# Performance work log

Measured on AMD Instinct MI355X. Metric: run time of the kernel, lower is better.

The kernel has to match this reference:

```python
import jax, jax.numpy as jnp
import numpy as np

NQ = 12          # num_qubits
NL = 5           # num_layers
NA = 4           # num_actions
DIM = 2 ** NQ    # state-vector dimension

# PennyLane convention: wire 0 is the most-significant bit of the state index.
_idx = np.arange(DIM)
_bits = (_idx[:, None] >> (NQ - 1 - np.arange(NQ))) & 1           # [DIM, NQ]
_cz = np.ones(DIM)
for _i in range(NQ):                                              # ring of CZs (all diagonal -> fuse)
    _cz *= np.where((_bits[:, _i] & _bits[:, (_i + 1) % NQ]) == 1, -1.0, 1.0)
CZ_RING = jnp.asarray(_cz, dtype=jnp.complex64)                   # [DIM]
ZTAB = jnp.asarray(1 - 2 * _bits[:, :NA], dtype=jnp.float32)      # [DIM, NA] PauliZ eigenvalues


def _bc(v):
    # broadcast an angle-derived scalar or [B] vector against [B, lead, trail]
    v = jnp.asarray(v)
    return v.reshape(v.shape + (1, 1))


def _apply_1q(state, wire, m00, m01, m10, m11):
    b = state.shape[0]
    lead, trail = 2 ** wire, 2 ** (NQ - 1 - wire)
    s = state.reshape(b, lead, 2, trail)
    s0, s1 = s[:, :, 0, :], s[:, :, 1, :]
    return jnp.stack([m00 * s0 + m01 * s1, m10 * s0 + m11 * s1], axis=2).reshape(b, DIM)


def _rx(state, wire, theta):
    c = _bc(jnp.cos(0.5 * theta)).astype(jnp.complex64)
    s = _bc(jnp.sin(0.5 * theta)).astype(jnp.complex64)
    return _apply_1q(state, wire, c, -1j * s, -1j * s, c)


def _ry(state, wire, theta):
    c = _bc(jnp.cos(0.5 * theta)).astype(jnp.complex64)
    s = _bc(jnp.sin(0.5 * theta)).astype(jnp.complex64)
    return _apply_1q(state, wire, c, -s, s, c)


def _rz(state, wire, theta):
    # diagonal gate: no mixing across the wire axis
    b = state.shape[0]
    lead, trail = 2 ** wire, 2 ** (NQ - 1 - wire)
    e = _bc(jnp.exp(-0.5j * theta))  # e^{-i t/2}; conj(e) = e^{+i t/2} for real t
    s = state.reshape(b, lead, 2, trail)
    return jnp.stack([e * s[:, :, 0, :], jnp.conj(e) * s[:, :, 1, :]], axis=2).reshape(b, DIM)


def setup_inputs() -> dict:
    key = jax.random.key(0)
    k1, k2 = jax.random.split(key)
    x = jax.random.normal(k1, (4096, 4 * NQ), dtype=jnp.float32)
    input_scaling = jnp.ones((NL, 3, NQ), dtype=jnp.float32)
    weights = jax.random.uniform(k2, (NL, 3, 2 * NQ), dtype=jnp.float32,
                                 minval=-np.pi, maxval=np.pi)
    output_scaling = jnp.ones((NA,), dtype=jnp.float32)
    return {"x": x, "input_scaling": input_scaling, "weights": weights,
            "output_scaling": output_scaling}


def reference(x, input_scaling, weights, output_scaling):
    b = x.shape[0]
    feats = (x[:, NQ:2 * NQ], x[:, 2 * NQ:3 * NQ], x[:, 3 * NQ:4 * NQ])
    state = jnp.zeros((b, DIM), dtype=jnp.complex64).at[:, 0].set(1.0)
    for layer in range(NL):
        for blk in range(3):
            f = feats[blk]
            for i in range(NQ):
                state = _rx(state, i, input_scaling[layer, blk, i] * f[:, i])
            for i in range(NQ):
                state = _ry(state, i, weights[layer, blk, i])
            for i in range(NQ):
                state = _rz(state, i, weights[layer, blk, i + NQ])
            state = state * CZ_RING[None, :]
    probs = state.real ** 2 + state.imag ** 2          # [B, DIM]
    expvals = probs @ ZTAB                             # [B, NA] <Z_i>
    return expvals * output_scaling                    # logits
```

## Files before the change

### kernel.cpp

```cpp
#include <hip/hip_runtime.h>
#include <stdint.h>

#define NQ 12
#define NL 5
#define NIT 15
#define AMPS 16
#define CPB (NIT * NQ)


typedef float f2 __attribute__((ext_vector_type(2)));

static __device__ __forceinline__ float f_u(unsigned u) { return __uint_as_float(u); }
static __device__ __forceinline__ unsigned u_f(float f) { return __float_as_uint(f); }

#define PK_MUL_RR(acc, C, S) \
    asm("v_pk_mul_f32 %0, %1, %2 op_sel_hi:[0,1]" : "=v"(acc) : "v"(C), "v"(S))
#define PK_FMA_I(acc, C, S) \
    asm("v_pk_fma_f32 %0, %1, %2, %0 op_sel:[1,1,0] op_sel_hi:[1,0,1] neg_lo:[1,0,0]" \
        : "+v"(acc) : "v"(C), "v"(S))
#define PK_FMA_R(acc, C, S) \
    asm("v_pk_fma_f32 %0, %1, %2, %0 op_sel_hi:[0,1,1]" : "+v"(acc) : "v"(C), "v"(S))
#define PK_FMA_IC(acc, C, S) \
    asm("v_pk_fma_f32 %0, %1, %2, %0 op_sel:[1,1,0] op_sel_hi:[1,0,1] neg_hi:[1,0,0]" \
        : "+v"(acc) : "v"(C), "v"(S))
#define PK_FMA_RN(acc, C, S) \
    asm("v_pk_fma_f32 %0, %1, %2, %0 op_sel_hi:[0,1,1] neg_lo:[1,0,0] neg_hi:[1,0,0]" \
        : "+v"(acc) : "v"(C), "v"(S))

#define CPLX_AB(DST, CA, S, CB, O)                                    \
    { f2 t_;                                                          \
      PK_MUL_RR(t_, CA, S); PK_FMA_I(t_, CA, S);                      \
      PK_FMA_R (t_, CB, O); PK_FMA_I(t_, CB, O);                      \
      DST = t_; }

template <int CTRL>
static __device__ __forceinline__ float dpp_xor(float v) {
    int u = (int)__float_as_uint(v);
    return __uint_as_float((unsigned)__builtin_amdgcn_update_dpp(u, u, CTRL, 0xF, 0xF, false));
}
static __device__ __forceinline__ float swz_xor4(float v) {
    return f_u((unsigned)__builtin_amdgcn_ds_swizzle((int)u_f(v), 0x101F));
}

#define AB_GATE_PK(OPX)                                                 \
    _Pragma("unroll")                                                   \
    for (int r = 0; r < AMPS; ++r) {                                    \
        f2 o; o.x = OPX(s[r].x); o.y = OPX(s[r].y);                     \
        CPLX_AB(s[r], CA, s[r], CB, o)                                  \
    }

template <int ST>
static __device__ __forceinline__ void reg_gate_pk(f2 (&s)[AMPS], f2 CAg, f2 CBg) {
#pragma unroll
    for (int r0 = 0; r0 < AMPS; ++r0) {
        if (r0 & ST) continue;
        const int r1 = r0 | ST;
        const f2 s0 = s[r0], s1 = s[r1];
        f2 t0, t1;
        PK_MUL_RR(t0, CAg, s0); PK_FMA_I (t0, CAg, s0);
        PK_FMA_R (t0, CBg, s1); PK_FMA_I (t0, CBg, s1);
        PK_MUL_RR(t1, CAg, s1); PK_FMA_IC(t1, CAg, s1);
        PK_FMA_RN(t1, CBg, s0); PK_FMA_I (t1, CBg, s0);
        s[r0] = t0; s[r1] = t1;
    }
}

static __device__ __forceinline__ float4 build_coef(float alpha, float beta, float gamma) {
    float sa, ca, sb, cb, sg, cg;
    sincosf(0.5f * alpha, &sa, &ca);
    sincosf(0.5f * beta,  &sb, &cb);
    sincosf(0.5f * gamma, &sg, &cg);
    float cbca = cb * ca, sbsa = sb * sa, sbca = sb * ca, cbsa = cb * sa;
    float ar =  cg * cbca + sg * sbsa;
    float ai =  cg * sbsa - sg * cbca;
    float br = -(cg * sbca + sg * cbsa);
    float bi =  sg * sbca - cg * cbsa;
    return make_float4(ar, ai, br, bi);
}

__global__ __launch_bounds__(256) void coef_kernel(
    const float* __restrict__ x, const float* __restrict__ iscale,
    const float* __restrict__ w, float4* __restrict__ ctab, int total)
{
    int gid = blockIdx.x * 256 + threadIdx.x;
    if (gid >= total) return;
    int b  = gid / CPB;
    int t  = gid - b * CPB;
    int it = t / NQ;
    int q  = t - it * NQ;
    int blk = it - 3 * (it / 3);
    float f     = x[(size_t)b * (4 * NQ) + NQ + blk * NQ + q];
    float alpha = iscale[it * NQ + q] * f;
    ctab[gid] = build_coef(alpha, w[it * 2 * NQ + q], w[it * 2 * NQ + NQ + q]);
}

template <bool TAB>
__global__ __launch_bounds__(256) void qsim_kernel(
    const float* __restrict__ x,
    const float* __restrict__ iscale,
    const float* __restrict__ w,
    const float* __restrict__ oscale,
    const float4* __restrict__ ctab,
    float* __restrict__ out)
{
    const int tid  = threadIdx.x;
    const int lane = tid & 63;
    const int wv   = tid >> 6;
    const int b    = blockIdx.x;

    extern __shared__ float4 smem[];
    float4* buf  = smem;
    float4* clds = smem + 1536;

#define TBUF(SLOT, Q) buf[((((SLOT) << 1) | (Q)) << 6) | lane]

    if constexpr (!TAB) {
        if (tid < CPB) {
            const int it  = tid / NQ;
            const int q   = tid - it * NQ;
            const int blk = it - 3 * (it / 3);
            float f     = x[(size_t)b * (4 * NQ) + NQ + blk * NQ + q];
            float alpha = iscale[it * NQ + q] * f;
            clds[tid] = build_coef(alpha, w[it * 2 * NQ + q], w[it * 2 * NQ + NQ + q]);
        }
        __syncthreads();
    }

    f2 s[AMPS];
#pragma unroll
    for (int r = 0; r < AMPS; ++r) { s[r].x = 0.f; s[r].y = 0.f; }
    if (tid == 0) s[0].x = 1.f;

    unsigned czmA = 0, czmB = 0;
#pragma unroll
    for (int r = 0; r < AMPS; ++r) {
        unsigned ia = ((unsigned)wv << 10) | ((unsigned)lane << 4) | (unsigned)r;
        unsigned ib = (((unsigned)(r >> 3) & 1u) << 11) | (((unsigned)(r >> 2) & 1u) << 10)
                    | ((unsigned)lane << 4)
                    | (((unsigned)(wv >> 1) & 1u) << 3) | (((unsigned)wv & 1u) << 2)
                    | ((unsigned)r & 3u);
        unsigned pa = ((unsigned)__popc((ia & (ia >> 1)) & 0x7FFu) + ((ia & (ia >> 11)) & 1u)) & 1u;
        unsigned pb = ((unsigned)__popc((ib & (ib >> 1)) & 0x7FFu) + ((ib & (ib >> 11)) & 1u)) & 1u;
        czmA |= pa << r;
        czmB |= pb << r;
    }

    const bool hb2 = (lane >> 5) & 1;
    const bool hb3 = (lane >> 4) & 1;
    const unsigned sb4 = (unsigned)((lane >> 3) & 1) << 31;
    const unsigned sb5 = (unsigned)((lane >> 2) & 1) << 31;
    const unsigned sb6 = (unsigned)((lane >> 1) & 1) << 31;
    const unsigned sb7 = (unsigned)(lane & 1) << 31;

    const float4* gtab = TAB ? (ctab + (size_t)b * CPB) : nullptr;

    float4 c[NQ];
    if constexpr (TAB) {
#pragma unroll
        for (int q = 0; q < NQ; ++q) c[q] = gtab[q];
    } else {
#pragma unroll
        for (int q = 0; q < NQ; ++q) c[q] = clds[q];
    }

#pragma unroll 1
    for (int it = 0; it < NIT; ++it) {
        float4 cn[NQ];
        if constexpr (TAB) {
            const float4* nxt = gtab + (it + 1 < NIT ? (it + 1) * NQ : it * NQ);
#pragma unroll
            for (int q = 0; q < NQ; ++q) cn[q] = nxt[q];
        } else {
            const float4* nxt = clds + (it + 1 < NIT ? (it + 1) * NQ : it * NQ);
#pragma unroll
            for (int q = 0; q < NQ; ++q) cn[q] = nxt[q];
        }

        const bool ev = (it & 1) == 0;

        {
            const float4 c0 = ev ? c[8] : c[0];
            const float4 c1 = ev ? c[9] : c[1];
            { const f2 CA = { c0.x, c0.y }, CB = { c0.z, c0.w }; reg_gate_pk<8>(s, CA, CB); }
            { const f2 CA = { c1.x, c1.y }, CB = { c1.z, c1.w }; reg_gate_pk<4>(s, CA, CB); }
            { const f2 CA = { c[10].x, c[10].y }, CB = { c[10].z, c[10].w }; reg_gate_pk<2>(s, CA, CB); }
            { const f2 CA = { c[11].x, c[11].y }, CB = { c[11].z, c[11].w }; reg_gate_pk<1>(s, CA, CB); }
        }

        {
            const f2 CP = { hb2 ? -c[2].z : c[2].x, hb2 ?  c[2].w : c[2].y };
            const f2 CQ = { hb2 ?  c[2].x : c[2].z, hb2 ? -c[2].y : c[2].w };
#pragma unroll
            for (int r = 0; r < AMPS; ++r) {
                auto dx = __builtin_amdgcn_permlane32_swap(u_f(s[r].x), u_f(s[r].x), false, false);
                auto dy = __builtin_amdgcn_permlane32_swap(u_f(s[r].y), u_f(s[r].y), false, false);
                f2 na = { f_u(dx[0]), f_u(dy[0]) };
                f2 nb = { f_u(dx[1]), f_u(dy[1]) };
                CPLX_AB(s[r], CP, na, CQ, nb)
            }
        }
        {
            const f2 CP = { hb3 ? -c[3].z : c[3].x, hb3 ?  c[3].w : c[3].y };
            const f2 CQ = { hb3 ?  c[3].x : c[3].z, hb3 ? -c[3].y : c[3].w };
#pragma unroll
            for (int r = 0; r < AMPS; ++r) {
                auto dx = __builtin_amdgcn_permlane16_swap(u_f(s[r].x), u_f(s[r].x), false, false);
                auto dy = __builtin_amdgcn_permlane16_swap(u_f(s[r].y), u_f(s[r].y), false, false);
                f2 na = { f_u(dx[0]), f_u(dy[0]) };
                f2 nb = { f_u(dx[1]), f_u(dy[1]) };
                CPLX_AB(s[r], CP, na, CQ, nb)
            }
        }
        {
            const f2 CA = { c[4].x, f_u(u_f(c[4].y) ^ sb4) };
            const f2 CB = { f_u(u_f(c[4].z) ^ sb4), c[4].w };
            AB_GATE_PK(dpp_xor<0x128>)
        }
        {
            const f2 CA = { c[5].x, f_u(u_f(c[5].y) ^ sb5) };
            const f2 CB = { f_u(u_f(c[5].z) ^ sb5), c[5].w };
            float ox[AMPS], oy[AMPS];
#pragma unroll
            for (int r = 0; r < AMPS; ++r) {
                ox[r] = swz_xor4(s[r].x);
                oy[r] = swz_xor4(s[r].y);
            }
#pragma unroll
            for (int r = 0; r < AMPS; ++r) {
                f2 o = { ox[r], oy[r] };
                CPLX_AB(s[r], CA, s[r], CB, o)
            }
        }
        {
            const f2 CA = { c[6].x, f_u(u_f(c[6].y) ^ sb6) };
            const f2 CB = { f_u(u_f(c[6].z) ^ sb6), c[6].w };
            AB_GATE_PK(dpp_xor<0x4E>)
        }
        {
            const f2 CA = { c[7].x, f_u(u_f(c[7].y) ^ sb7) };
            const f2 CB = { f_u(u_f(c[7].z) ^ sb7), c[7].w };
            AB_GATE_PK(dpp_xor<0xB1>)
        }

        __syncthreads();
#pragma unroll
        for (int g = 0; g < 4; ++g) {
            if (g == wv) continue;
            const int slot = g * 3 + (wv < g ? wv : wv - 1);
            TBUF(slot, 0) = make_float4(s[4*g+0].x, s[4*g+0].y, s[4*g+1].x, s[4*g+1].y);
            TBUF(slot, 1) = make_float4(s[4*g+2].x, s[4*g+2].y, s[4*g+3].x, s[4*g+3].y);
        }
        __syncthreads();
#pragma unroll
        for (int h = 0; h < 4; ++h) {
            if (h == wv) continue;
            const int slot = wv * 3 + (h < wv ? h : h - 1);
            const float4 pa = TBUF(slot, 0);
            const float4 pb = TBUF(slot, 1);
            s[4*h+0] = f2{ pa.x, pa.y }; s[4*h+1] = f2{ pa.z, pa.w };
            s[4*h+2] = f2{ pb.x, pb.y }; s[4*h+3] = f2{ pb.z, pb.w };
        }

        {
            const float4 c0 = ev ? c[0] : c[8];
            const float4 c1 = ev ? c[1] : c[9];
            { const f2 CA = { c0.x, c0.y }, CB = { c0.z, c0.w }; reg_gate_pk<8>(s, CA, CB); }
            { const f2 CA = { c1.x, c1.y }, CB = { c1.z, c1.w }; reg_gate_pk<4>(s, CA, CB); }
        }

        const unsigned mcz = ev ? czmB : czmA;
#pragma unroll
        for (int r = 0; r < AMPS; ++r) {
            const unsigned sgn = ((mcz >> r) & 1u) << 31;
            s[r].x = f_u(u_f(s[r].x) ^ sgn);
            s[r].y = f_u(u_f(s[r].y) ^ sgn);
        }

#pragma unroll
        for (int q = 0; q < NQ; ++q) c[q] = cn[q];
    }

    float pg[4];
#pragma unroll
    for (int g = 0; g < 4; ++g) {
        float p = 0.f;
#pragma unroll
        for (int j = 0; j < 4; ++j)
            p = fmaf(s[4*g+j].x, s[4*g+j].x, fmaf(s[4*g+j].y, s[4*g+j].y, p));
        pg[g] = p;
    }
    const float ptot = (pg[0] + pg[1]) + (pg[2] + pg[3]);
    float v0 = (pg[0] + pg[1]) - (pg[2] + pg[3]);
    float v1 = (pg[0] + pg[2]) - (pg[1] + pg[3]);
    float v2 = hb2 ? -ptot : ptot;
    float v3 = hb3 ? -ptot : ptot;
#pragma unroll
    for (int m = 1; m <= 32; m <<= 1) {
        v0 += __shfl_xor(v0, m);
        v1 += __shfl_xor(v1, m);
        v2 += __shfl_xor(v2, m);
        v3 += __shfl_xor(v3, m);
    }

    __syncthreads();
    if (lane == 0) buf[wv] = make_float4(v0, v1, v2, v3);
    __syncthreads();
    if (tid == 0) {
        float4 a0 = buf[0], a1 = buf[1], a2 = buf[2], a3 = buf[3];
        float4 o;
        o.x = (a0.x + a1.x + a2.x + a3.x) * oscale[0];
        o.y = (a0.y + a1.y + a2.y + a3.y) * oscale[1];
        o.z = (a0.z + a1.z + a2.z + a3.z) * oscale[2];
        o.w = (a0.w + a1.w + a2.w + a3.w) * oscale[3];
        *reinterpret_cast<float4*>(out + (size_t)b * 4) = o;
    }
#undef TBUF
}

extern "C" void kernel_launch(void* const* d_in, const int* in_sizes, int n_in,
                              void* d_out, int out_size, void* d_ws, size_t ws_size,
                              hipStream_t stream) {
    const float* x      = (const float*)d_in[0];
    const float* iscale = (const float*)d_in[1];
    const float* w      = (const float*)d_in[2];
    const float* oscale = (const float*)d_in[3];
    float* out          = (float*)d_out;

    const int batch = in_sizes[0] / (4 * NQ);
    const size_t need = (size_t)batch * CPB * sizeof(float4);

    if (ws_size >= need) {
        const int total = batch * CPB;
        coef_kernel<<<(total + 255) / 256, 256, 0, stream>>>(x, iscale, w, (float4*)d_ws, total);
        qsim_kernel<true><<<batch, 256, 12 * 2 * 64 * sizeof(float4), stream>>>(
            x, iscale, w, oscale, (const float4*)d_ws, out);
    } else {
        qsim_kernel<false><<<batch, 256, (12 * 2 * 64 + CPB) * sizeof(float4), stream>>>(
            x, iscale, w, oscale, nullptr, out);
    }
}
```

Baseline: 568.4 us.

## Fold first iteration into analytic product state and drop coefficient prepass kernel

The separate coefficient kernel and its global workspace table are removed. Each block now computes gate coefficients into LDS itself. The first iteration, which starts from |0…0>, no longer simulates gates: the product state is built directly as a tensor product of per-qubit amplitude columns via complex multiplies, then the CZ signs are applied. The main loop starts at iteration 1, reads coefficients from LDS each iteration instead of prefetching them in registers, and is unrolled by 2. This removes a kernel launch, the global traffic, and one iteration of gate and exchange work, at the cost of per-block sincos work before the first barrier.

```diff
diff --git a/kernel.cpp b/kernel.cpp
--- a/kernel.cpp
+++ b/kernel.cpp
@@ -27,6 +27,9 @@
     asm("v_pk_fma_f32 %0, %1, %2, %0 op_sel_hi:[0,1,1] neg_lo:[1,0,0] neg_hi:[1,0,0]" \
         : "+v"(acc) : "v"(C), "v"(S))
 
+#define CMUL(DST, CA, CB) \
+    { PK_MUL_RR(DST, CA, CB); PK_FMA_I(DST, CA, CB); }
+
 #define CPLX_AB(DST, CA, S, CB, O)                                    \
     { f2 t_;                                                          \
       PK_MUL_RR(t_, CA, S); PK_FMA_I(t_, CA, S);                      \
@@ -78,29 +81,11 @@
     return make_float4(ar, ai, br, bi);
 }
 
-__global__ __launch_bounds__(256) void coef_kernel(
-    const float* __restrict__ x, const float* __restrict__ iscale,
-    const float* __restrict__ w, float4* __restrict__ ctab, int total)
-{
-    int gid = blockIdx.x * 256 + threadIdx.x;
-    if (gid >= total) return;
-    int b  = gid / CPB;
-    int t  = gid - b * CPB;
-    int it = t / NQ;
-    int q  = t - it * NQ;
-    int blk = it - 3 * (it / 3);
-    float f     = x[(size_t)b * (4 * NQ) + NQ + blk * NQ + q];
-    float alpha = iscale[it * NQ + q] * f;
-    ctab[gid] = build_coef(alpha, w[it * 2 * NQ + q], w[it * 2 * NQ + NQ + q]);
-}
-
-template <bool TAB>
 __global__ __launch_bounds__(256) void qsim_kernel(
     const float* __restrict__ x,
     const float* __restrict__ iscale,
     const float* __restrict__ w,
     const float* __restrict__ oscale,
-    const float4* __restrict__ ctab,
     float* __restrict__ out)
 {
     const int tid  = threadIdx.x;
@@ -108,28 +93,19 @@
     const int wv   = tid >> 6;
     const int b    = blockIdx.x;
 
-    extern __shared__ float4 smem[];
-    float4* buf  = smem;
-    float4* clds = smem + 1536;
+    __shared__ float4 buf[1536];
+    __shared__ float4 clds[CPB];
 
 #define TBUF(SLOT, Q) buf[((((SLOT) << 1) | (Q)) << 6) | lane]
 
-    if constexpr (!TAB) {
-        if (tid < CPB) {
-            const int it  = tid / NQ;
-            const int q   = tid - it * NQ;
-            const int blk = it - 3 * (it / 3);
-            float f     = x[(size_t)b * (4 * NQ) + NQ + blk * NQ + q];
-            float alpha = iscale[it * NQ + q] * f;
-            clds[tid] = build_coef(alpha, w[it * 2 * NQ + q], w[it * 2 * NQ + NQ + q]);
-        }
-        __syncthreads();
-    }
-
-    f2 s[AMPS];
-#pragma unroll
-    for (int r = 0; r < AMPS; ++r) { s[r].x = 0.f; s[r].y = 0.f; }
-    if (tid == 0) s[0].x = 1.f;
+    if (tid < CPB) {
+        const int it  = tid / NQ;
+        const int q   = tid - it * NQ;
+        const int blk = it - 3 * (it / 3);
+        float f     = x[(size_t)b * (4 * NQ) + NQ + blk * NQ + q];
+        float alpha = iscale[it * NQ + q] * f;
+        clds[tid] = build_coef(alpha, w[it * 2 * NQ + q], w[it * 2 * NQ + NQ + q]);
+    }
 
     unsigned czmA = 0, czmB = 0;
 #pragma unroll
@@ -152,30 +128,62 @@
     const unsigned sb6 = (unsigned)((lane >> 1) & 1) << 31;
     const unsigned sb7 = (unsigned)(lane & 1) << 31;
 
-    const float4* gtab = TAB ? (ctab + (size_t)b * CPB) : nullptr;
-
-    float4 c[NQ];
-    if constexpr (TAB) {
-#pragma unroll
-        for (int q = 0; q < NQ; ++q) c[q] = gtab[q];
-    } else {
+    __syncthreads();
+
+    f2 s[AMPS];
+
+    {
+        float4 c[NQ];
 #pragma unroll
         for (int q = 0; q < NQ; ++q) c[q] = clds[q];
-    }
-
-#pragma unroll 1
-    for (int it = 0; it < NIT; ++it) {
-        float4 cn[NQ];
-        if constexpr (TAB) {
-            const float4* nxt = gtab + (it + 1 < NIT ? (it + 1) * NQ : it * NQ);
-#pragma unroll
-            for (int q = 0; q < NQ; ++q) cn[q] = nxt[q];
-        } else {
-            const float4* nxt = clds + (it + 1 < NIT ? (it + 1) * NQ : it * NQ);
-#pragma unroll
-            for (int q = 0; q < NQ; ++q) cn[q] = nxt[q];
-        }
-
+
+        f2 tc;
+        {
+            const int b2 = (lane >> 5) & 1;
+            tc = b2 ? f2{ -c[2].z, c[2].w } : f2{ c[2].x, c[2].y };
+#pragma unroll
+            for (int wq = 3; wq <= 7; ++wq) {
+                const int bit = (lane >> (7 - wq)) & 1;
+                const f2 uw = bit ? f2{ -c[wq].z, c[wq].w } : f2{ c[wq].x, c[wq].y };
+                f2 t; CMUL(t, tc, uw); tc = t;
+            }
+            const int b8 = (wv >> 1) & 1;
+            const f2 u8 = b8 ? f2{ -c[8].z, c[8].w } : f2{ c[8].x, c[8].y };
+            { f2 t; CMUL(t, tc, u8); tc = t; }
+            const int b9 = wv & 1;
+            const f2 u9 = b9 ? f2{ -c[9].z, c[9].w } : f2{ c[9].x, c[9].y };
+            { f2 t; CMUL(t, tc, u9); tc = t; }
+        }
+
+        f2 ph[4], pl[4];
+        {
+            const f2 a0 = { c[0].x, c[0].y }, a1 = { -c[0].z, c[0].w };
+            const f2 b0 = { c[1].x, c[1].y }, b1 = { -c[1].z, c[1].w };
+            CMUL(ph[0], a0, b0) CMUL(ph[1], a0, b1)
+            CMUL(ph[2], a1, b0) CMUL(ph[3], a1, b1)
+#pragma unroll
+            for (int j = 0; j < 4; ++j) { f2 t; CMUL(t, tc, ph[j]); ph[j] = t; }
+            const f2 g0 = { c[10].x, c[10].y }, g1 = { -c[10].z, c[10].w };
+            const f2 h0 = { c[11].x, c[11].y }, h1 = { -c[11].z, c[11].w };
+            CMUL(pl[0], g0, h0) CMUL(pl[1], g0, h1)
+            CMUL(pl[2], g1, h0) CMUL(pl[3], g1, h1)
+        }
+#pragma unroll
+        for (int r = 0; r < AMPS; ++r) CMUL(s[r], ph[r >> 2], pl[r & 3])
+
+#pragma unroll
+        for (int r = 0; r < AMPS; ++r) {
+            const unsigned sgn = ((czmB >> r) & 1u) << 31;
+            s[r].x = f_u(u_f(s[r].x) ^ sgn);
+            s[r].y = f_u(u_f(s[r].y) ^ sgn);
+        }
+    }
+
+#pragma unroll 2
+    for (int it = 1; it < NIT; ++it) {
+        float4 c[NQ];
+#pragma unroll
+        for (int q = 0; q < NQ; ++q) c[q] = clds[it * NQ + q];
         const bool ev = (it & 1) == 0;
 
         {
@@ -275,9 +283,6 @@
             s[r].x = f_u(u_f(s[r].x) ^ sgn);
             s[r].y = f_u(u_f(s[r].y) ^ sgn);
         }
-
-#pragma unroll
-        for (int q = 0; q < NQ; ++q) c[q] = cn[q];
     }
 
     float pg[4];
@@ -327,15 +332,5 @@
     float* out          = (float*)d_out;
 
     const int batch = in_sizes[0] / (4 * NQ);
-    const size_t need = (size_t)batch * CPB * sizeof(float4);
-
-    if (ws_size >= need) {
-        const int total = batch * CPB;
-        coef_kernel<<<(total + 255) / 256, 256, 0, stream>>>(x, iscale, w, (float4*)d_ws, total);
-        qsim_kernel<true><<<batch, 256, 12 * 2 * 64 * sizeof(float4), stream>>>(
-            x, iscale, w, oscale, (const float4*)d_ws, out);
-    } else {
-        qsim_kernel<false><<<batch, 256, (12 * 2 * 64 + CPB) * sizeof(float4), stream>>>(
-            x, iscale, w, oscale, nullptr, out);
-    }
-}
+    qsim_kernel<<<batch, 256, 0, stream>>>(x, iscale, w, oscale, out);
+}
```

Result: faster. 513.6 us (-9.6%).

## Compute first iteration analytically as product state, drop coefficient prefetch

Applied to the files above, without the earlier changes.

Because the initial state is |0…0>, the state after the first block of single-qubit gates is a product state. The kernel now builds each amplitude directly as a product of per-qubit coefficient columns, then applies the CZ sign, instead of running the full gate and exchange sequence for iteration 0. The main loop starts at iteration 1, loads coefficients directly rather than double-buffering them, and is unrolled by 2. The coefficient kernel is relaunched with one block per batch element. This removes one of 15 iterations of gate and shuffle work but adds some complex multiplies and register pressure from the unroll.

```diff
diff --git a/kernel.cpp b/kernel.cpp
--- a/kernel.cpp
+++ b/kernel.cpp
@@ -2,7 +2,6 @@
 #include <stdint.h>
 
 #define NQ 12
-#define NL 5
 #define NIT 15
 #define AMPS 16
 #define CPB (NIT * NQ)
@@ -27,6 +26,9 @@
     asm("v_pk_fma_f32 %0, %1, %2, %0 op_sel_hi:[0,1,1] neg_lo:[1,0,0] neg_hi:[1,0,0]" \
         : "+v"(acc) : "v"(C), "v"(S))
 
+#define CMUL(DST, CA, CB) \
+    { PK_MUL_RR(DST, CA, CB); PK_FMA_I(DST, CA, CB); }
+
 #define CPLX_AB(DST, CA, S, CB, O)                                    \
     { f2 t_;                                                          \
       PK_MUL_RR(t_, CA, S); PK_FMA_I(t_, CA, S);                      \
@@ -78,20 +80,25 @@
     return make_float4(ar, ai, br, bi);
 }
 
+static __device__ __forceinline__ f2 usel(float4 c, int bit) {
+    return bit ? f2{ -c.z, c.w } : f2{ c.x, c.y };
+}
+
 __global__ __launch_bounds__(256) void coef_kernel(
     const float* __restrict__ x, const float* __restrict__ iscale,
-    const float* __restrict__ w, float4* __restrict__ ctab, int total)
+    const float* __restrict__ w, float4* __restrict__ ctab)
 {
-    int gid = blockIdx.x * 256 + threadIdx.x;
-    if (gid >= total) return;
-    int b  = gid / CPB;
-    int t  = gid - b * CPB;
-    int it = t / NQ;
-    int q  = t - it * NQ;
-    int blk = it - 3 * (it / 3);
-    float f     = x[(size_t)b * (4 * NQ) + NQ + blk * NQ + q];
-    float alpha = iscale[it * NQ + q] * f;
-    ctab[gid] = build_coef(alpha, w[it * 2 * NQ + q], w[it * 2 * NQ + NQ + q]);
+    const int b = blockIdx.x;
+    const int t = threadIdx.x;
+    if (t < CPB) {
+        const int it  = t / NQ;
+        const int q   = t - it * NQ;
+        const int blk = it - 3 * (it / 3);
+        float f     = x[(size_t)b * (4 * NQ) + NQ + blk * NQ + q];
+        float alpha = iscale[it * NQ + q] * f;
+        ctab[(size_t)b * CPB + t] =
+            build_coef(alpha, w[it * 2 * NQ + q], w[it * 2 * NQ + NQ + q]);
+    }
 }
 
 template <bool TAB>
@@ -123,13 +130,7 @@
             float alpha = iscale[it * NQ + q] * f;
             clds[tid] = build_coef(alpha, w[it * 2 * NQ + q], w[it * 2 * NQ + NQ + q]);
         }
-        __syncthreads();
-    }
-
-    f2 s[AMPS];
-#pragma unroll
-    for (int r = 0; r < AMPS; ++r) { s[r].x = 0.f; s[r].y = 0.f; }
-    if (tid == 0) s[0].x = 1.f;
+    }
 
     unsigned czmA = 0, czmB = 0;
 #pragma unroll
@@ -154,28 +155,59 @@
 
     const float4* gtab = TAB ? (ctab + (size_t)b * CPB) : nullptr;
 
-    float4 c[NQ];
-    if constexpr (TAB) {
-#pragma unroll
-        for (int q = 0; q < NQ; ++q) c[q] = gtab[q];
-    } else {
-#pragma unroll
-        for (int q = 0; q < NQ; ++q) c[q] = clds[q];
-    }
-
-#pragma unroll 1
-    for (int it = 0; it < NIT; ++it) {
-        float4 cn[NQ];
+    if constexpr (!TAB) __syncthreads();
+
+    f2 s[AMPS];
+
+    {
+        float4 c[NQ];
         if constexpr (TAB) {
-            const float4* nxt = gtab + (it + 1 < NIT ? (it + 1) * NQ : it * NQ);
-#pragma unroll
-            for (int q = 0; q < NQ; ++q) cn[q] = nxt[q];
+#pragma unroll
+            for (int q = 0; q < NQ; ++q) c[q] = gtab[q];
         } else {
-            const float4* nxt = clds + (it + 1 < NIT ? (it + 1) * NQ : it * NQ);
-#pragma unroll
-            for (int q = 0; q < NQ; ++q) cn[q] = nxt[q];
-        }
-
+#pragma unroll
+            for (int q = 0; q < NQ; ++q) c[q] = clds[q];
+        }
+
+        f2 tc = usel(c[2], (lane >> 5) & 1);
+#pragma unroll
+        for (int wq = 3; wq <= 7; ++wq) {
+            const f2 uw = usel(c[wq], (lane >> (7 - wq)) & 1);
+            f2 t; CMUL(t, tc, uw) tc = t;
+        }
+        { f2 u = usel(c[8], (wv >> 1) & 1); f2 t; CMUL(t, tc, u) tc = t; }
+        { f2 u = usel(c[9], wv & 1);        f2 t; CMUL(t, tc, u) tc = t; }
+
+        f2 ph[4], pl[4];
+#pragma unroll
+        for (int j = 0; j < 4; ++j) {
+            f2 u0 = usel(c[0], j >> 1), u1 = usel(c[1], j & 1);
+            CMUL(ph[j], u0, u1)
+            f2 t; CMUL(t, tc, ph[j]) ph[j] = t;
+            f2 uA = usel(c[10], j >> 1), uB = usel(c[11], j & 1);
+            CMUL(pl[j], uA, uB)
+        }
+#pragma unroll
+        for (int r = 0; r < AMPS; ++r) CMUL(s[r], ph[r >> 2], pl[r & 3])
+
+#pragma unroll
+        for (int r = 0; r < AMPS; ++r) {
+            const unsigned sgn = ((czmB >> r) & 1u) << 31;
+            s[r].x = f_u(u_f(s[r].x) ^ sgn);
+            s[r].y = f_u(u_f(s[r].y) ^ sgn);
+        }
+    }
+
+#pragma unroll 2
+    for (int it = 1; it < NIT; ++it) {
+        float4 c[NQ];
+        if constexpr (TAB) {
+#pragma unroll
+            for (int q = 0; q < NQ; ++q) c[q] = gtab[it * NQ + q];
+        } else {
+#pragma unroll
+            for (int q = 0; q < NQ; ++q) c[q] = clds[it * NQ + q];
+        }
         const bool ev = (it & 1) == 0;
 
         {
@@ -275,9 +307,6 @@
             s[r].x = f_u(u_f(s[r].x) ^ sgn);
             s[r].y = f_u(u_f(s[r].y) ^ sgn);
         }
-
-#pragma unroll
-        for (int q = 0; q < NQ; ++q) c[q] = cn[q];
     }
 
     float pg[4];
@@ -330,12 +359,11 @@
     const size_t need = (size_t)batch * CPB * sizeof(float4);
 
     if (ws_size >= need) {
-        const int total = batch * CPB;
-        coef_kernel<<<(total + 255) / 256, 256, 0, stream>>>(x, iscale, w, (float4*)d_ws, total);
-        qsim_kernel<true><<<batch, 256, 12 * 2 * 64 * sizeof(float4), stream>>>(
+        coef_kernel<<<batch, 256, 0, stream>>>(x, iscale, w, (float4*)d_ws);
+        qsim_kernel<true><<<batch, 256, 1536 * sizeof(float4), stream>>>(
             x, iscale, w, oscale, (const float4*)d_ws, out);
     } else {
-        qsim_kernel<false><<<batch, 256, (12 * 2 * 64 + CPB) * sizeof(float4), stream>>>(
+        qsim_kernel<false><<<batch, 256, (1536 + CPB) * sizeof(float4), stream>>>(
             x, iscale, w, oscale, nullptr, out);
     }
 }
```

New measurement: 520.8 us. -8.4%, faster.
